# Kernel tuning notes

Measured on AMD Instinct MI355X. Metric: run time of the kernel, lower is better.

The kernel has to match this reference:

```python
import jax, jax.numpy as jnp
import numpy as np
import math

B, L, D = 2, 2048, 768
H, R = 12, 128
DH = D // H  # 64

def setup_inputs():
    key = jax.random.key(0)
    ks = jax.random.split(key, 9)
    s = 0.02
    return {
        "x": jax.random.normal(ks[0], (B, L, D), jnp.float32),
        "W_qkv": jax.random.normal(ks[1], (D, 3 * D), jnp.float32) * s,
        "b_qkv": jnp.zeros((3 * D,), jnp.float32),
        "W_sem_down": jax.random.normal(ks[2], (D, R), jnp.float32) * s,
        "W_sem_up": jax.random.normal(ks[3], (R, 2 * D), jnp.float32) * s,
        "W_ctx_down": jax.random.normal(ks[4], (D, R), jnp.float32) * s,
        "W_ctx_up": jax.random.normal(ks[5], (R, 2 * D), jnp.float32) * s,
        "temperature": jnp.ones((1,), jnp.float32) * 0.5,
        "W_proj": jax.random.normal(ks[6], (D, D), jnp.float32) * s,
        "b_proj": jnp.zeros((D,), jnp.float32),
        "gamma": jnp.ones((D,), jnp.float32),
        "beta": jnp.zeros((D,), jnp.float32),
    }

def _layernorm(x, gamma, beta, eps=1e-5):
    mu = x.mean(-1, keepdims=True)
    var = ((x - mu) ** 2).mean(-1, keepdims=True)
    return (x - mu) * jax.lax.rsqrt(var + eps) * gamma + beta

def reference(x, W_qkv, b_qkv, W_sem_down, W_sem_up, W_ctx_down, W_ctx_up,
              temperature, W_proj, b_proj, gamma, beta):
    x_norm = _layernorm(x, gamma, beta)
    qkv = x_norm @ W_qkv + b_qkv
    q, k, v = jnp.split(qkv, 3, axis=-1)

    # sinusoidal interference gate from two low-rank branches
    sem = jax.nn.silu(x @ W_sem_down) @ W_sem_up
    sem_amp, sem_phase = jnp.split(sem, 2, axis=-1)
    sem_amp = jax.nn.softplus(sem_amp)
    sem_phase = jnp.tanh(sem_phase) * math.pi
    ctx = jax.nn.silu(x @ W_ctx_down) @ W_ctx_up
    ctx_amp, ctx_phase = jnp.split(ctx, 2, axis=-1)
    ctx_amp = jax.nn.softplus(ctx_amp)
    ctx_phase = jnp.tanh(ctx_phase) * math.pi
    interference = sem_amp * ctx_amp * jnp.cos(sem_phase - ctx_phase) * temperature
    gate = jax.nn.sigmoid(interference)
    k = k * (1.0 + gate)

    # (B,L,D) -> (B,H,L,DH)
    to_heads = lambda t: t.reshape(B, L, H, DH).transpose(0, 2, 1, 3)
    q_f = jax.nn.elu(to_heads(q).astype(jnp.float32)) + 1.0
    k_f = jax.nn.elu(to_heads(k).astype(jnp.float32)) + 1.0
    v_f = to_heads(v).astype(jnp.float32)

    # causal linear attention via explicit k (x) v cumsum
    kv_state = k_f[..., :, None] * v_f[..., None, :]   # (B,H,L,DH,DH)
    kv_cumsum = jnp.cumsum(kv_state, axis=2)
    out_num = jnp.einsum('bhld,bhlde->bhle', q_f, kv_cumsum)
    k_cumsum = jnp.cumsum(k_f, axis=2)
    out_den = (q_f * k_cumsum).sum(-1, keepdims=True) + 1e-6
    attn = (out_num / out_den).astype(x.dtype)
    attn = attn.transpose(0, 2, 1, 3).reshape(B, L, D)
    return attn @ W_proj + b_proj, gate
```

## Files before the change

### kernel.cpp

```cpp
#include <hip/hip_runtime.h>

#define B_    2
#define L_    2048
#define D_    768
#define H_    12
#define BL    4096
#define BH    24
#define CHUNK 128
#define NC    16
#define GOFF  3145728
#define PI_F  3.14159265358979f

typedef __bf16 bf16x8 __attribute__((ext_vector_type(8)));
typedef float  f32x4  __attribute__((ext_vector_type(4)));
typedef unsigned short us8 __attribute__((ext_vector_type(8)));

__device__ __forceinline__ float bf2f(unsigned short u) {
    return __uint_as_float(((unsigned int)u) << 16);
}
__device__ __forceinline__ unsigned short f2bf(float f) {
    unsigned int u = __float_as_uint(f);
    unsigned int r = (u + 0x7fffu + ((u >> 16) & 1u)) >> 16;
    return (unsigned short)r;
}
__device__ __forceinline__ float rcp_fast(float x) { return __builtin_amdgcn_rcpf(x); }
__device__ __forceinline__ float softplus_fast(float x) {
    return x > 20.f ? x : __logf(1.f + __expf(x));
}
__device__ __forceinline__ float tanh_fast(float x) {
    float e2 = __expf(2.f * x);
    return 1.f - 2.f * rcp_fast(e2 + 1.f);
}
__device__ __forceinline__ void dma16(const unsigned short* g, unsigned short* l) {
    __builtin_amdgcn_global_load_lds(
        (const __attribute__((address_space(1))) unsigned int*)g,
        (__attribute__((address_space(3))) unsigned int*)l, 16, 0, 0);
}

__global__ __launch_bounds__(256) void detect_kernel(const unsigned short* __restrict__ x,
                                                     int* __restrict__ flag)
{
    __shared__ int cnt;
    if (threadIdx.x == 0) cnt = 0;
    __syncthreads();
    int c = 0;
    #pragma unroll
    for (int i = 0; i < 16; i++) {
        unsigned short u = x[threadIdx.x * 16 + i];
        int e = (u >> 7) & 0xff;
        if (e < 100 || e > 140) c++;
    }
    atomicAdd(&cnt, c);
    __syncthreads();
    if (threadIdx.x == 0) flag[0] = (cnt > 512) ? 1 : 0;
}

__global__ __launch_bounds__(256) void prep_mega_kernel(
    const void* __restrict__ s0, unsigned short* __restrict__ dq,
    const void* __restrict__ s1, unsigned short* __restrict__ dd,
    const void* __restrict__ s2, unsigned short* __restrict__ dsu,
    const void* __restrict__ s3,
    const void* __restrict__ s4, unsigned short* __restrict__ dcu,
    const void* __restrict__ s5, unsigned short* __restrict__ dp,
    const void* __restrict__ sbq, unsigned short* __restrict__ dbq,
    const void* __restrict__ sbp, unsigned short* __restrict__ dbp,
    const int* __restrict__ flag)
{
    int id = blockIdx.x;
    int fl = flag[0];
    if (id >= 2880) {
        const void* src; unsigned short* dst; int n, base;
        if (id < 2889) { src = sbq; dst = dbq; n = 2304; base = (id - 2880) * 256; }
        else           { src = sbp; dst = dbp; n = 768;  base = (id - 2889) * 256; }
        int i = base + threadIdx.x;
        if (i < n) dst[i] = fl ? f2bf(((const float*)src)[i]) : ((const unsigned short*)src)[i];
        return;
    }
    __shared__ unsigned short tile[32][33];
    const void* src; unsigned short* dst; int K, N, tid;
    if (id < 1728)      { src = s0; dst = dq;  K = 768; N = 2304; tid = id; }
    else if (id < 1824) { src = s1; dst = dd;  K = 768; N = 128;  tid = id - 1728; }
    else if (id < 2016) { src = s2; dst = dsu; K = 128; N = 1536; tid = id - 1824; }
    else if (id < 2112) { src = s3; dst = dd + (size_t)128 * 768; K = 768; N = 128; tid = id - 2016; }
    else if (id < 2304) { src = s4; dst = dcu; K = 128; N = 1536; tid = id - 2112; }
    else                { src = s5; dst = dp;  K = 768; N = 768;  tid = id - 2304; }
    int tn = N / 32;
    int by = (tid / tn) * 32, bx = (tid % tn) * 32;
    int tx = threadIdx.x & 31, tyb = threadIdx.x >> 5;
    #pragma unroll
    for (int i = 0; i < 4; i++) {
        int k = by + tyb * 4 + i, n = bx + tx;
        size_t off = (size_t)k * N + n;
        tile[tyb * 4 + i][tx] = fl ? f2bf(((const float*)src)[off]) : ((const unsigned short*)src)[off];
    }
    __syncthreads();
    #pragma unroll
    for (int i = 0; i < 4; i++) {
        int n = bx + tyb * 4 + i, k = by + tx;
        dst[(size_t)n * K + k] = tile[tx][tyb * 4 + i];
    }
}

__global__ __launch_bounds__(256) void conv_ln_kernel(
    const void* __restrict__ xin,
    const void* __restrict__ gr, const void* __restrict__ br,
    unsigned short* __restrict__ x_c,
    unsigned short* __restrict__ xn,
    const int* __restrict__ flag)
{
    int row = blockIdx.x, t = threadIdx.x;
    int fl = flag[0];
    float v[3];
    #pragma unroll
    for (int j = 0; j < 3; j++) {
        int c = t + j * 256;
        v[j] = fl ? ((const float*)xin)[(size_t)row * D_ + c]
                  : bf2f(((const unsigned short*)xin)[(size_t)row * D_ + c]);
    }
    __shared__ float red[8];
    float s = v[0] + v[1] + v[2];
    #pragma unroll
    for (int m = 32; m >= 1; m >>= 1) s += __shfl_xor(s, m, 64);
    int wid = t >> 6;
    if ((t & 63) == 0) red[wid] = s;
    __syncthreads();
    float mean = (red[0] + red[1] + red[2] + red[3]) * (1.f / 768.f);
    float s2 = 0.f;
    #pragma unroll
    for (int j = 0; j < 3; j++) { float d = v[j] - mean; s2 += d * d; }
    #pragma unroll
    for (int m = 32; m >= 1; m >>= 1) s2 += __shfl_xor(s2, m, 64);
    if ((t & 63) == 0) red[4 + wid] = s2;
    __syncthreads();
    float var = (red[4] + red[5] + red[6] + red[7]) * (1.f / 768.f);
    float rs = rsqrtf(var + 1e-5f);
    #pragma unroll
    for (int j = 0; j < 3; j++) {
        int c = t + j * 256;
        float gv = fl ? ((const float*)gr)[c] : bf2f(((const unsigned short*)gr)[c]);
        float bv = fl ? ((const float*)br)[c] : bf2f(((const unsigned short*)br)[c]);
        x_c[(size_t)row * D_ + c] = f2bf(v[j]);
        float o = (v[j] - mean) * rs * gv + bv;
        xn[(size_t)row * D_ + c] = f2bf(o);
    }
}

template<int EPI>
__global__ __launch_bounds__(256) void mfma_gemm_kernel(
    const unsigned short* __restrict__ A, int lda,
    const unsigned short* __restrict__ BT,
    const unsigned short* __restrict__ bias,
    const unsigned short* __restrict__ gateb,
    void* __restrict__ outp,
    const int* __restrict__ flag,
    int N, int K)
{
    __shared__ unsigned short sbuf[17408];
    unsigned short* As = sbuf;
    unsigned short* Bs = sbuf + 8192;
    unsigned short* Cs = sbuf;

    int f = blockIdx.y * gridDim.x + blockIdx.x;
    int rps = gridDim.y >> 3;
    int strip = f & 7, within = f >> 3;
    int by = strip * rps + (within % rps);
    int bx = within / rps;
    int m0 = by * 128, n0 = bx * 128;

    int t = threadIdx.x;
    int lane = t & 63, wave = t >> 6, quad = lane >> 4, l16 = lane & 15;
    int wm = (wave & 1) * 64, wn = (wave >> 1) * 64;
    int xr = l16 & 7;

    int sr8 = lane >> 3;
    int scg = (lane & 7) ^ sr8;
    const unsigned short* ApL = A  + (size_t)(m0 + wave * 32 + sr8) * lda + scg * 8;
    const unsigned short* BpL = BT + (size_t)(n0 + wave * 32 + sr8) * K   + scg * 8;
    unsigned short* AsW = As + wave * 32 * 64;
    unsigned short* BsW = Bs + wave * 32 * 64;

    f32x4 acc[4][4];
    #pragma unroll
    for (int i = 0; i < 4; i++)
        #pragma unroll
        for (int j = 0; j < 4; j++) acc[i][j] = (f32x4){0.f, 0.f, 0.f, 0.f};

    for (int k0 = 0; k0 < K; k0 += 64) {
        __syncthreads();
        #pragma unroll
        for (int c = 0; c < 4; c++) {
            dma16(ApL + (size_t)(c * 8) * lda + k0, AsW + c * 512);
            dma16(BpL + (size_t)(c * 8) * K   + k0, BsW + c * 512);
        }
        __syncthreads();
        #pragma unroll
        for (int ks = 0; ks < 2; ks++) {
            bf16x8 af[4], bfr[4];
            #pragma unroll
            for (int i = 0; i < 4; i++)
                af[i] = *(const bf16x8*)&As[(wm + i * 16 + l16) * 64 + (((ks * 4 + quad) ^ xr) * 8)];
            #pragma unroll
            for (int j = 0; j < 4; j++)
                bfr[j] = *(const bf16x8*)&Bs[(wn + j * 16 + l16) * 64 + (((ks * 4 + quad) ^ xr) * 8)];
            #pragma unroll
            for (int i = 0; i < 4; i++)
                #pragma unroll
                for (int j = 0; j < 4; j++)
                    acc[i][j] = __builtin_amdgcn_mfma_f32_16x16x32_bf16(af[i], bfr[j], acc[i][j], 0, 0, 0);
        }
    }

    int fl = (EPI == 3) ? flag[0] : 0;
    __syncthreads();
    #pragma unroll
    for (int j = 0; j < 4; j++) {
        int col = n0 + wn + j * 16 + l16;
        float bv = bias ? bf2f(bias[col]) : 0.f;
        #pragma unroll
        for (int i = 0; i < 4; i++) {
            #pragma unroll
            for (int r = 0; r < 4; r++) {
                int row = m0 + wm + i * 16 + quad * 4 + r;
                float v = acc[i][j][r] + bv;
                if (EPI == 1) v = v * rcp_fast(1.f + __expf(-v));
                if (EPI == 2) {
                    if (col < D_) {
                        v = v > 0.f ? v + 1.f : __expf(v);
                    } else if (col < 2 * D_) {
                        float gg = bf2f(gateb[(size_t)row * D_ + (col - D_)]);
                        v *= (1.f + gg);
                        v = v > 0.f ? v + 1.f : __expf(v);
                    }
                }
                if (EPI == 3 && fl) {
                    ((float*)outp)[(size_t)row * N + col] = v;
                } else {
                    Cs[(wm + i * 16 + quad * 4 + r) * 136 + wn + j * 16 + l16] = f2bf(v);
                }
            }
        }
    }
    if (!(EPI == 3 && fl)) {
        __syncthreads();
        #pragma unroll
        for (int p = 0; p < 8; p++) {
            int idx = p * 256 + t;
            int row = idx >> 4, cc = (idx & 15) * 8;
            *(us8*)&((unsigned short*)outp)[(size_t)(m0 + row) * N + n0 + cc] =
                *(const us8*)&Cs[row * 136 + cc];
        }
    }
}

__global__ __launch_bounds__(256) void gate_mfma_kernel(
    const unsigned short* __restrict__ tdown,
    const unsigned short* __restrict__ WsuT,
    const unsigned short* __restrict__ WcuT,
    const void* __restrict__ tempraw,
    void* __restrict__ dout,
    unsigned short* __restrict__ gateb,
    const int* __restrict__ flag)
{
    __shared__ unsigned short gbuf[17408];
    int f = blockIdx.y * gridDim.x + blockIdx.x;
    int rps = gridDim.y >> 3;
    int strip = f & 7, within = f >> 3;
    int by = strip * rps + (within % rps);
    int bx = within / rps;
    int m0 = by * 64, c0 = bx * 64;

    int t = threadIdx.x;
    int lane = t & 63, wave = t >> 6, quad = lane >> 4, l16 = lane & 15;
    int xg = l16 & 3;

    int r_t = wave * 16 + (lane >> 2);
    int g_t = (lane & 3) ^ ((lane >> 2) & 3);
    const unsigned short* s0 = tdown + (size_t)(m0 + r_t) * 256 + g_t * 8;
    const unsigned short* s1 = s0 + 128;
    const unsigned short* s2 = WsuT + (size_t)(c0 + r_t) * 128 + g_t * 8;
    const unsigned short* s3 = WsuT + (size_t)(768 + c0 + r_t) * 128 + g_t * 8;
    const unsigned short* s4 = WcuT + (size_t)(c0 + r_t) * 128 + g_t * 8;
    const unsigned short* s5 = WcuT + (size_t)(768 + c0 + r_t) * 128 + g_t * 8;
    unsigned short* ldq = gbuf + wave * 512;

    f32x4 acc[4][4];
    #pragma unroll
    for (int i = 0; i < 4; i++)
        #pragma unroll
        for (int j = 0; j < 4; j++) acc[i][j] = (f32x4){0.f, 0.f, 0.f, 0.f};

    int Atile = wave >> 1, Btile = 2 + wave;
    for (int k0 = 0; k0 < 128; k0 += 32) {
        __syncthreads();
        dma16(s0 + k0, ldq + 0 * 2048);
        dma16(s1 + k0, ldq + 1 * 2048);
        dma16(s2 + k0, ldq + 2 * 2048);
        dma16(s3 + k0, ldq + 3 * 2048);
        dma16(s4 + k0, ldq + 4 * 2048);
        dma16(s5 + k0, ldq + 5 * 2048);
        __syncthreads();
        bf16x8 af[4], bfr[4];
        #pragma unroll
        for (int i = 0; i < 4; i++)
            af[i] = *(const bf16x8*)&gbuf[Atile * 2048 + (i * 16 + l16) * 32 + ((quad ^ xg) * 8)];
        #pragma unroll
        for (int j = 0; j < 4; j++)
            bfr[j] = *(const bf16x8*)&gbuf[Btile * 2048 + (j * 16 + l16) * 32 + ((quad ^ xg) * 8)];
        #pragma unroll
        for (int i = 0; i < 4; i++)
            #pragma unroll
            for (int j = 0; j < 4; j++)
                acc[i][j] = __builtin_amdgcn_mfma_f32_16x16x32_bf16(af[i], bfr[j], acc[i][j], 0, 0, 0);
    }
    __syncthreads();
    #pragma unroll
    for (int i = 0; i < 4; i++)
        #pragma unroll
        for (int j = 0; j < 4; j++)
            #pragma unroll
            for (int r = 0; r < 4; r++)
                gbuf[wave * 4352 + (i * 16 + quad * 4 + r) * 68 + j * 16 + l16] = f2bf(acc[i][j][r]);
    __syncthreads();
    int fl = flag[0];
    float tempv = fl ? ((const float*)tempraw)[0] : bf2f(((const unsigned short*)tempraw)[0]);
    #pragma unroll
    for (int p = 0; p < 16; p++) {
        int idx = p * 256 + t;
        int row = idx >> 6, col = idx & 63;
        float sa = softplus_fast(bf2f(gbuf[0 * 4352 + row * 68 + col]));
        float sp = tanh_fast(bf2f(gbuf[1 * 4352 + row * 68 + col]));
        float ca = softplus_fast(bf2f(gbuf[2 * 4352 + row * 68 + col]));
        float cp = tanh_fast(bf2f(gbuf[3 * 4352 + row * 68 + col]));
        float inter = sa * ca * __cosf(PI_F * (sp - cp)) * tempv;
        float g = rcp_fast(1.f + __expf(-inter));
        size_t off = (size_t)GOFF + (size_t)(m0 + row) * D_ + c0 + col;
        unsigned short gb = f2bf(g);
        if (fl) ((float*)dout)[off] = g;
        else    ((unsigned short*)dout)[off] = gb;
        gateb[(size_t)(m0 + row) * D_ + c0 + col] = gb;
    }
}

__global__ __launch_bounds__(256) void chunk_sum_mfma_kernel(
    const unsigned short* __restrict__ qkvt,
    float* __restrict__ Msum, float* __restrict__ Zsum)
{
    __shared__ __align__(16) unsigned short KT[64 * 136];
    __shared__ __align__(16) unsigned short VT[80 * 136];
    int blk = blockIdx.x;
    int bh = blk / NC, cc = blk - bh * NC;
    int b = bh / H_, h = bh - b * H_;
    int t = threadIdx.x;
    int lane = t & 63, wave = t >> 6, quad = lane >> 4, l16 = lane & 15;
    int lr = t >> 1, lc = (t & 1) * 32;
    size_t rowbase = (size_t)(b * L_ + cc * CHUNK);
    const unsigned short* kg = qkvt + rowbase * 2304 + D_ + h * 64;
    const unsigned short* vg = qkvt + rowbase * 2304 + 2 * D_ + h * 64;
    #pragma unroll
    for (int c = 0; c < 4; c++) {
        us8 kv = *(const us8*)&kg[(size_t)lr * 2304 + lc + c * 8];
        us8 vv = *(const us8*)&vg[(size_t)lr * 2304 + lc + c * 8];
        #pragma unroll
        for (int ii = 0; ii < 8; ii++) {
            KT[(lc + c * 8 + ii) * 136 + lr] = kv[ii];
            VT[(lc + c * 8 + ii) * 136 + lr] = vv[ii];
        }
    }
    if (t < 128) VT[64 * 136 + t] = 0x3F80;
    __syncthreads();

    f32x4 acc[5];
    #pragma unroll
    for (int j = 0; j < 5; j++) acc[j] = (f32x4){0.f, 0.f, 0.f, 0.f};
    #pragma unroll
    for (int ks = 0; ks < 4; ks++) {
        bf16x8 a = *(const bf16x8*)&KT[(wave * 16 + l16) * 136 + ks * 32 + quad * 8];
        #pragma unroll
        for (int j = 0; j < 5; j++) {
            bf16x8 bv = *(const bf16x8*)&VT[(j * 16 + l16) * 136 + ks * 32 + quad * 8];
            acc[j] = __builtin_amdgcn_mfma_f32_16x16x32_bf16(a, bv, acc[j], 0, 0, 0);
        }
    }
    float* mo = Msum + (size_t)blk * 4096;
    #pragma unroll
    for (int j = 0; j < 4; j++)
        #pragma unroll
        for (int r = 0; r < 4; r++)
            mo[(wave * 16 + quad * 4 + r) * 64 + j * 16 + l16] = acc[j][r];
    if (l16 == 0) {
        #pragma unroll
        for (int r = 0; r < 4; r++)
            Zsum[(size_t)blk * 64 + wave * 16 + quad * 4 + r] = acc[4][r];
    }
}

__global__ __launch_bounds__(256) void chunk_scan_mfma_kernel(
    const unsigned short* __restrict__ qkvt,
    const float* __restrict__ Msum, const float* __restrict__ Zsum,
    unsigned short* __restrict__ attnb)
{
    __shared__ __align__(16) unsigned short sbuf[34048];
    unsigned short* Qs = sbuf;
    unsigned short* Ks = sbuf + 8192;
    unsigned short* Ps = sbuf;
    unsigned short* VT = sbuf + 17408;
    unsigned short* Ss = sbuf + 28288;
    unsigned short* Cout = sbuf;

    int blk = blockIdx.x;
    int bh = blk / NC, cc = NC - 1 - (blk - bh * NC);
    int b = bh / H_, h = bh - b * H_;
    int t = threadIdx.x;
    int lane = t & 63, wave = t >> 6, quad = lane >> 4, l16 = lane & 15;
    int wm = wave * 32;
    int xr = l16 & 7;
    size_t rowbase = (size_t)(b * L_ + cc * CHUNK);
    const unsigned short* qg = qkvt + rowbase * 2304 + h * 64;
    const unsigned short* kg = qkvt + rowbase * 2304 + D_ + h * 64;
    const unsigned short* vg = qkvt + rowbase * 2304 + 2 * D_ + h * 64;

    int r8 = lane >> 3, g8 = (lane & 7) ^ r8;
    #pragma unroll
    for (int s = 0; s < 8; s++) {
        int op = s * 4 + wave;
        int tl = op >> 4, o16 = op & 15;
        const unsigned short* src = (tl ? kg : qg) + (size_t)(o16 * 8 + r8) * 2304 + g8 * 8;
        unsigned short* dst = (tl ? Ks : Qs) + o16 * 512;
        dma16(src, dst);
    }
    {
        int lr = t >> 1, lc = (t & 1) * 32;
        #pragma unroll
        for (int c = 0; c < 4; c++) {
            us8 vv = *(const us8*)&vg[(size_t)lr * 2304 + lc + c * 8];
            #pragma unroll
            for (int ii = 0; ii < 8; ii++)
                VT[(lc + c * 8 + ii) * 136 + lr] = vv[ii];
        }
    }
    if (t < 128) VT[64 * 136 + t] = 0x3F80;
    {
        int d = t & 63, jb = (t >> 6) * 16;
        float a16[16];
        #pragma unroll
        for (int j = 0; j < 16; j++) a16[j] = 0.f;
        for (int c = 0; c < cc; c++) {
            const float* mp = Msum + ((size_t)bh * NC + c) * 4096 + d * 64 + jb;
            #pragma unroll
            for (int g4 = 0; g4 < 4; g4++) {
                float4 sv = *(const float4*)&mp[g4 * 4];
                a16[g4 * 4 + 0] += sv.x; a16[g4 * 4 + 1] += sv.y;
                a16[g4 * 4 + 2] += sv.z; a16[g4 * 4 + 3] += sv.w;
            }
        }
        #pragma unroll
        for (int j = 0; j < 16; j++) Ss[(jb + j) * 72 + d] = f2bf(a16[j]);
    }
    if (t < 64) {
        float rz = 0.f;
        for (int c = 0; c < cc; c++) rz += Zsum[((size_t)bh * NC + c) * 64 + t];
        Ss[64 * 72 + t] = f2bf(rz);
    }
    __syncthreads();

    f32x4 Pacc[2][8], Oacc[2][5];
    #pragma unroll
    for (int i = 0; i < 2; i++) {
        #pragma unroll
        for (int n = 0; n < 8; n++) Pacc[i][n] = (f32x4){0.f, 0.f, 0.f, 0.f};
        #pragma unroll
        for (int j = 0; j < 5; j++) Oacc[i][j] = (f32x4){0.f, 0.f, 0.f, 0.f};
    }
    bf16x8 aq[2][2];
    #pragma unroll
    for (int i = 0; i < 2; i++)
        #pragma unroll
        for (int ks = 0; ks < 2; ks++)
            aq[i][ks] = *(const bf16x8*)&Qs[(wm + i * 16 + l16) * 64 + (((ks * 4 + quad) ^ xr) * 8)];
    #pragma unroll
    for (int n = 0; n < 8; n++)
        #pragma unroll
        for (int ks = 0; ks < 2; ks++) {
            bf16x8 bk = *(const bf16x8*)&Ks[(n * 16 + l16) * 64 + (((ks * 4 + quad) ^ xr) * 8)];
            #pragma unroll
            for (int i = 0; i < 2; i++)
                Pacc[i][n] = __builtin_amdgcn_mfma_f32_16x16x32_bf16(aq[i][ks], bk, Pacc[i][n], 0, 0, 0);
        }
    #pragma unroll
    for (int j = 0; j < 5; j++)
        #pragma unroll
        for (int ks = 0; ks < 2; ks++) {
            bf16x8 bs = *(const bf16x8*)&Ss[(j * 16 + l16) * 72 + ks * 32 + quad * 8];
            #pragma unroll
            for (int i = 0; i < 2; i++)
                Oacc[i][j] = __builtin_amdgcn_mfma_f32_16x16x32_bf16(aq[i][ks], bs, Oacc[i][j], 0, 0, 0);
        }
    __syncthreads();

    #pragma unroll
    for (int i = 0; i < 2; i++)
        #pragma unroll
        for (int n = 0; n < 8; n++)
            #pragma unroll
            for (int r = 0; r < 4; r++) {
                int trow = wm + i * 16 + quad * 4 + r;
                int scol = n * 16 + l16;
                Ps[trow * 136 + scol] = (scol <= trow) ? f2bf(Pacc[i][n][r]) : 0;
            }
    __syncthreads();

    #pragma unroll
    for (int ks = 0; ks < 4; ks++) {
        bf16x8 ap[2];
        #pragma unroll
        for (int i = 0; i < 2; i++)
            ap[i] = *(const bf16x8*)&Ps[(wm + i * 16 + l16) * 136 + ks * 32 + quad * 8];
        #pragma unroll
        for (int j = 0; j < 5; j++) {
            bf16x8 bv = *(const bf16x8*)&VT[(j * 16 + l16) * 136 + ks * 32 + quad * 8];
            #pragma unroll
            for (int i = 0; i < 2; i++)
                Oacc[i][j] = __builtin_amdgcn_mfma_f32_16x16x32_bf16(ap[i], bv, Oacc[i][j], 0, 0, 0);
        }
    }
    __syncthreads();

    #pragma unroll
    for (int i = 0; i < 2; i++) {
        #pragma unroll
        for (int r = 0; r < 4; r++) {
            float den = __shfl(Oacc[i][4][r], lane & 48) + 1e-6f;
            float inv = 1.f / den;
            #pragma unroll
            for (int j = 0; j < 4; j++)
                Cout[(wm + i * 16 + quad * 4 + r) * 136 + j * 16 + l16] = f2bf(Oacc[i][j][r] * inv);
        }
    }
    __syncthreads();
    unsigned short* abase = attnb + rowbase * D_ + h * 64;
    #pragma unroll
    for (int p = 0; p < 4; p++) {
        int idx = p * 256 + t;
        int row = idx >> 3, cg = (idx & 7) * 8;
        *(us8*)&abase[(size_t)row * D_ + cg] = *(const us8*)&Cout[row * 136 + cg];
    }
}

extern "C" void kernel_launch(void* const* d_in, const int* in_sizes, int n_in,
                              void* d_out, int out_size, void* d_ws, size_t ws_size,
                              hipStream_t stream)
{
    char* w = (char*)d_ws;
    auto alloc = [&](size_t bytes) { void* p = (void*)w; w += (bytes + 255) & ~(size_t)255; return p; };
    int*            flagp   = (int*)alloc(256);
    unsigned short* x_c     = (unsigned short*)alloc((size_t)BL * D_ * 2);
    unsigned short* attnb   = x_c;
    unsigned short* xn      = (unsigned short*)alloc((size_t)BL * D_ * 2);
    unsigned short* WqkvT   = (unsigned short*)alloc((size_t)2304 * 768 * 2);
    unsigned short* WdT     = (unsigned short*)alloc((size_t)256 * 768 * 2);
    unsigned short* WsuT    = (unsigned short*)alloc((size_t)1536 * 128 * 2);
    unsigned short* WcuT    = (unsigned short*)alloc((size_t)1536 * 128 * 2);
    unsigned short* WprojT  = (unsigned short*)alloc((size_t)768 * 768 * 2);
    unsigned short* bqkv_c  = (unsigned short*)alloc((size_t)2304 * 2);
    unsigned short* bproj_c = (unsigned short*)alloc((size_t)768 * 2);
    unsigned short* tdown   = (unsigned short*)alloc((size_t)BL * 256 * 2);
    float*          Zsum    = (float*)alloc((size_t)BH * NC * 64 * 4);
    unsigned short* qkvt    = (unsigned short*)alloc((size_t)BL * 2304 * 2);
    float*          Msum    = (float*)alloc((size_t)BH * NC * 4096 * 4);
    unsigned short* gateb   = (unsigned short*)Msum;

    dim3 blk(256);
    detect_kernel<<<1, blk, 0, stream>>>((const unsigned short*)d_in[0], flagp);
    prep_mega_kernel<<<2892, blk, 0, stream>>>(
        d_in[1], WqkvT, d_in[3], WdT, d_in[4], WsuT,
        d_in[5], d_in[6], WcuT, d_in[8], WprojT,
        d_in[2], bqkv_c, d_in[9], bproj_c, flagp);
    conv_ln_kernel<<<BL, blk, 0, stream>>>(d_in[0], d_in[10], d_in[11], x_c, xn, flagp);
    mfma_gemm_kernel<1><<<dim3(2, 32), blk, 0, stream>>>(x_c, 768, WdT, nullptr, nullptr, tdown, flagp, 256, 768);
    gate_mfma_kernel<<<dim3(12, 64), blk, 0, stream>>>(tdown, WsuT, WcuT, d_in[7], d_out, gateb, flagp);
    mfma_gemm_kernel<2><<<dim3(18, 32), blk, 0, stream>>>(xn, 768, WqkvT, bqkv_c, gateb, qkvt, flagp, 2304, 768);
    chunk_sum_mfma_kernel<<<BH * NC, blk, 0, stream>>>(qkvt, Msum, Zsum);
    chunk_scan_mfma_kernel<<<BH * NC, blk, 0, stream>>>(qkvt, Msum, Zsum, attnb);
    mfma_gemm_kernel<3><<<dim3(6, 32), blk, 0, stream>>>(attnb, 768, WprojT, bproj_c, nullptr, d_out, flagp, 768, 768);
}
```

Baseline: 225.2 us.

## Fuse dtype detection, weight prep and layernorm into one launch; use 64-row GEMM tiles

Merges the separate detect, weight-transpose and layernorm kernels into a single launch. Each block recomputes the dtype flag locally from a smaller sample of x, which removes two launches and their serial dependencies. The GEMM kernel gains an M-tile template parameter, and the small-N GEMMs (down-projection and output projection) now use 64-row tiles to double their block counts for better CU occupancy. The trade-off is that every block repeats the detection read and barrier, and the smaller sample makes the dtype heuristic less robust.

After: 220.9 us. Within noise of the previous version (-1.9%).

```diff
diff --git a/kernel.cpp b/kernel.cpp
--- a/kernel.cpp
+++ b/kernel.cpp
@@ -36,26 +36,23 @@
         (const __attribute__((address_space(1))) unsigned int*)g,
         (__attribute__((address_space(3))) unsigned int*)l, 16, 0, 0);
 }
-
-__global__ __launch_bounds__(256) void detect_kernel(const unsigned short* __restrict__ x,
-                                                     int* __restrict__ flag)
-{
-    __shared__ int cnt;
-    if (threadIdx.x == 0) cnt = 0;
+__device__ __forceinline__ int detect_local(const unsigned short* __restrict__ x,
+                                            int* cnt_sh) {
+    if (threadIdx.x == 0) *cnt_sh = 0;
     __syncthreads();
     int c = 0;
     #pragma unroll
-    for (int i = 0; i < 16; i++) {
-        unsigned short u = x[threadIdx.x * 16 + i];
+    for (int i = 0; i < 4; i++) {
+        unsigned short u = x[threadIdx.x * 4 + i];
         int e = (u >> 7) & 0xff;
         if (e < 100 || e > 140) c++;
     }
-    atomicAdd(&cnt, c);
-    __syncthreads();
-    if (threadIdx.x == 0) flag[0] = (cnt > 512) ? 1 : 0;
-}
-
-__global__ __launch_bounds__(256) void prep_mega_kernel(
+    atomicAdd(cnt_sh, c);
+    __syncthreads();
+    return *cnt_sh > 128;
+}
+
+__global__ __launch_bounds__(256) void prep_all_kernel(
     const void* __restrict__ s0, unsigned short* __restrict__ dq,
     const void* __restrict__ s1, unsigned short* __restrict__ dd,
     const void* __restrict__ s2, unsigned short* __restrict__ dsu,
@@ -64,19 +61,63 @@
     const void* __restrict__ s5, unsigned short* __restrict__ dp,
     const void* __restrict__ sbq, unsigned short* __restrict__ dbq,
     const void* __restrict__ sbp, unsigned short* __restrict__ dbp,
-    const int* __restrict__ flag)
+    const void* __restrict__ xin,
+    const void* __restrict__ gr, const void* __restrict__ br,
+    unsigned short* __restrict__ x_c, unsigned short* __restrict__ xn,
+    int* __restrict__ flagp)
 {
+    __shared__ int cnt_sh;
+    __shared__ unsigned short tile[32][33];
+    __shared__ float red[8];
+    int fl = detect_local((const unsigned short*)xin, &cnt_sh);
     int id = blockIdx.x;
-    int fl = flag[0];
+    int t = threadIdx.x;
+
+    if (id >= 2892) {
+        int row = id - 2892;
+        if (row == 0 && t == 0) flagp[0] = fl;
+        float v[3];
+        #pragma unroll
+        for (int j = 0; j < 3; j++) {
+            int c = t + j * 256;
+            v[j] = fl ? ((const float*)xin)[(size_t)row * D_ + c]
+                      : bf2f(((const unsigned short*)xin)[(size_t)row * D_ + c]);
+        }
+        float s = v[0] + v[1] + v[2];
+        #pragma unroll
+        for (int m = 32; m >= 1; m >>= 1) s += __shfl_xor(s, m, 64);
+        int wid = t >> 6;
+        if ((t & 63) == 0) red[wid] = s;
+        __syncthreads();
+        float mean = (red[0] + red[1] + red[2] + red[3]) * (1.f / 768.f);
+        float s2 = 0.f;
+        #pragma unroll
+        for (int j = 0; j < 3; j++) { float d = v[j] - mean; s2 += d * d; }
+        #pragma unroll
+        for (int m = 32; m >= 1; m >>= 1) s2 += __shfl_xor(s2, m, 64);
+        if ((t & 63) == 0) red[4 + wid] = s2;
+        __syncthreads();
+        float var = (red[4] + red[5] + red[6] + red[7]) * (1.f / 768.f);
+        float rs = rsqrtf(var + 1e-5f);
+        #pragma unroll
+        for (int j = 0; j < 3; j++) {
+            int c = t + j * 256;
+            float gv = fl ? ((const float*)gr)[c] : bf2f(((const unsigned short*)gr)[c]);
+            float bv = fl ? ((const float*)br)[c] : bf2f(((const unsigned short*)br)[c]);
+            x_c[(size_t)row * D_ + c] = f2bf(v[j]);
+            float o = (v[j] - mean) * rs * gv + bv;
+            xn[(size_t)row * D_ + c] = f2bf(o);
+        }
+        return;
+    }
     if (id >= 2880) {
         const void* src; unsigned short* dst; int n, base;
         if (id < 2889) { src = sbq; dst = dbq; n = 2304; base = (id - 2880) * 256; }
         else           { src = sbp; dst = dbp; n = 768;  base = (id - 2889) * 256; }
-        int i = base + threadIdx.x;
+        int i = base + t;
         if (i < n) dst[i] = fl ? f2bf(((const float*)src)[i]) : ((const unsigned short*)src)[i];
         return;
     }
-    __shared__ unsigned short tile[32][33];
     const void* src; unsigned short* dst; int K, N, tid;
     if (id < 1728)      { src = s0; dst = dq;  K = 768; N = 2304; tid = id; }
     else if (id < 1824) { src = s1; dst = dd;  K = 768; N = 128;  tid = id - 1728; }
@@ -86,7 +127,7 @@
     else                { src = s5; dst = dp;  K = 768; N = 768;  tid = id - 2304; }
     int tn = N / 32;
     int by = (tid / tn) * 32, bx = (tid % tn) * 32;
-    int tx = threadIdx.x & 31, tyb = threadIdx.x >> 5;
+    int tx = t & 31, tyb = t >> 5;
     #pragma unroll
     for (int i = 0; i < 4; i++) {
         int k = by + tyb * 4 + i, n = bx + tx;
@@ -101,51 +142,7 @@
     }
 }
 
-__global__ __launch_bounds__(256) void conv_ln_kernel(
-    const void* __restrict__ xin,
-    const void* __restrict__ gr, const void* __restrict__ br,
-    unsigned short* __restrict__ x_c,
-    unsigned short* __restrict__ xn,
-    const int* __restrict__ flag)
-{
-    int row = blockIdx.x, t = threadIdx.x;
-    int fl = flag[0];
-    float v[3];
-    #pragma unroll
-    for (int j = 0; j < 3; j++) {
-        int c = t + j * 256;
-        v[j] = fl ? ((const float*)xin)[(size_t)row * D_ + c]
-                  : bf2f(((const unsigned short*)xin)[(size_t)row * D_ + c]);
-    }
-    __shared__ float red[8];
-    float s = v[0] + v[1] + v[2];
-    #pragma unroll
-    for (int m = 32; m >= 1; m >>= 1) s += __shfl_xor(s, m, 64);
-    int wid = t >> 6;
-    if ((t & 63) == 0) red[wid] = s;
-    __syncthreads();
-    float mean = (red[0] + red[1] + red[2] + red[3]) * (1.f / 768.f);
-    float s2 = 0.f;
-    #pragma unroll
-    for (int j = 0; j < 3; j++) { float d = v[j] - mean; s2 += d * d; }
-    #pragma unroll
-    for (int m = 32; m >= 1; m >>= 1) s2 += __shfl_xor(s2, m, 64);
-    if ((t & 63) == 0) red[4 + wid] = s2;
-    __syncthreads();
-    float var = (red[4] + red[5] + red[6] + red[7]) * (1.f / 768.f);
-    float rs = rsqrtf(var + 1e-5f);
-    #pragma unroll
-    for (int j = 0; j < 3; j++) {
-        int c = t + j * 256;
-        float gv = fl ? ((const float*)gr)[c] : bf2f(((const unsigned short*)gr)[c]);
-        float bv = fl ? ((const float*)br)[c] : bf2f(((const unsigned short*)br)[c]);
-        x_c[(size_t)row * D_ + c] = f2bf(v[j]);
-        float o = (v[j] - mean) * rs * gv + bv;
-        xn[(size_t)row * D_ + c] = f2bf(o);
-    }
-}
-
-template<int EPI>
+template<int EPI, int TM>
 __global__ __launch_bounds__(256) void mfma_gemm_kernel(
     const unsigned short* __restrict__ A, int lda,
     const unsigned short* __restrict__ BT,
@@ -155,9 +152,11 @@
     const int* __restrict__ flag,
     int N, int K)
 {
+    constexpr int MI = TM / 32;
+    constexpr int AOPS = TM / 32;
     __shared__ unsigned short sbuf[17408];
     unsigned short* As = sbuf;
-    unsigned short* Bs = sbuf + 8192;
+    unsigned short* Bs = sbuf + TM * 64;
     unsigned short* Cs = sbuf;
 
     int f = blockIdx.y * gridDim.x + blockIdx.x;
@@ -165,45 +164,46 @@
     int strip = f & 7, within = f >> 3;
     int by = strip * rps + (within % rps);
     int bx = within / rps;
-    int m0 = by * 128, n0 = bx * 128;
+    int m0 = by * TM, n0 = bx * 128;
 
     int t = threadIdx.x;
     int lane = t & 63, wave = t >> 6, quad = lane >> 4, l16 = lane & 15;
-    int wm = (wave & 1) * 64, wn = (wave >> 1) * 64;
+    int wm = (wave & 1) * (TM / 2), wn = (wave >> 1) * 64;
     int xr = l16 & 7;
 
     int sr8 = lane >> 3;
     int scg = (lane & 7) ^ sr8;
-    const unsigned short* ApL = A  + (size_t)(m0 + wave * 32 + sr8) * lda + scg * 8;
+    const unsigned short* ApL = A  + (size_t)(m0 + wave * (TM / 4) + sr8) * lda + scg * 8;
     const unsigned short* BpL = BT + (size_t)(n0 + wave * 32 + sr8) * K   + scg * 8;
-    unsigned short* AsW = As + wave * 32 * 64;
+    unsigned short* AsW = As + wave * (TM / 4) * 64;
     unsigned short* BsW = Bs + wave * 32 * 64;
 
-    f32x4 acc[4][4];
-    #pragma unroll
-    for (int i = 0; i < 4; i++)
+    f32x4 acc[MI][4];
+    #pragma unroll
+    for (int i = 0; i < MI; i++)
         #pragma unroll
         for (int j = 0; j < 4; j++) acc[i][j] = (f32x4){0.f, 0.f, 0.f, 0.f};
 
     for (int k0 = 0; k0 < K; k0 += 64) {
         __syncthreads();
         #pragma unroll
-        for (int c = 0; c < 4; c++) {
+        for (int c = 0; c < AOPS; c++)
             dma16(ApL + (size_t)(c * 8) * lda + k0, AsW + c * 512);
-            dma16(BpL + (size_t)(c * 8) * K   + k0, BsW + c * 512);
-        }
+        #pragma unroll
+        for (int c = 0; c < 4; c++)
+            dma16(BpL + (size_t)(c * 8) * K + k0, BsW + c * 512);
         __syncthreads();
         #pragma unroll
         for (int ks = 0; ks < 2; ks++) {
-            bf16x8 af[4], bfr[4];
-            #pragma unroll
-            for (int i = 0; i < 4; i++)
+            bf16x8 af[MI], bfr[4];
+            #pragma unroll
+            for (int i = 0; i < MI; i++)
                 af[i] = *(const bf16x8*)&As[(wm + i * 16 + l16) * 64 + (((ks * 4 + quad) ^ xr) * 8)];
             #pragma unroll
             for (int j = 0; j < 4; j++)
                 bfr[j] = *(const bf16x8*)&Bs[(wn + j * 16 + l16) * 64 + (((ks * 4 + quad) ^ xr) * 8)];
             #pragma unroll
-            for (int i = 0; i < 4; i++)
+            for (int i = 0; i < MI; i++)
                 #pragma unroll
                 for (int j = 0; j < 4; j++)
                     acc[i][j] = __builtin_amdgcn_mfma_f32_16x16x32_bf16(af[i], bfr[j], acc[i][j], 0, 0, 0);
@@ -217,7 +217,7 @@
         int col = n0 + wn + j * 16 + l16;
         float bv = bias ? bf2f(bias[col]) : 0.f;
         #pragma unroll
-        for (int i = 0; i < 4; i++) {
+        for (int i = 0; i < MI; i++) {
             #pragma unroll
             for (int r = 0; r < 4; r++) {
                 int row = m0 + wm + i * 16 + quad * 4 + r;
@@ -243,7 +243,7 @@
     if (!(EPI == 3 && fl)) {
         __syncthreads();
         #pragma unroll
-        for (int p = 0; p < 8; p++) {
+        for (int p = 0; p < TM / 16; p++) {
             int idx = p * 256 + t;
             int row = idx >> 4, cc = (idx & 15) * 8;
             *(us8*)&((unsigned short*)outp)[(size_t)(m0 + row) * N + n0 + cc] =
@@ -570,16 +570,15 @@
     unsigned short* gateb   = (unsigned short*)Msum;
 
     dim3 blk(256);
-    detect_kernel<<<1, blk, 0, stream>>>((const unsigned short*)d_in[0], flagp);
-    prep_mega_kernel<<<2892, blk, 0, stream>>>(
+    prep_all_kernel<<<2892 + BL, blk, 0, stream>>>(
         d_in[1], WqkvT, d_in[3], WdT, d_in[4], WsuT,
         d_in[5], d_in[6], WcuT, d_in[8], WprojT,
-        d_in[2], bqkv_c, d_in[9], bproj_c, flagp);
-    conv_ln_kernel<<<BL, blk, 0, stream>>>(d_in[0], d_in[10], d_in[11], x_c, xn, flagp);
-    mfma_gemm_kernel<1><<<dim3(2, 32), blk, 0, stream>>>(x_c, 768, WdT, nullptr, nullptr, tdown, flagp, 256, 768);
+        d_in[2], bqkv_c, d_in[9], bproj_c,
+        d_in[0], d_in[10], d_in[11], x_c, xn, flagp);
+    mfma_gemm_kernel<1, 64><<<dim3(2, 64), blk, 0, stream>>>(x_c, 768, WdT, nullptr, nullptr, tdown, flagp, 256, 768);
     gate_mfma_kernel<<<dim3(12, 64), blk, 0, stream>>>(tdown, WsuT, WcuT, d_in[7], d_out, gateb, flagp);
-    mfma_gemm_kernel<2><<<dim3(18, 32), blk, 0, stream>>>(xn, 768, WqkvT, bqkv_c, gateb, qkvt, flagp, 2304, 768);
+    mfma_gemm_kernel<2, 128><<<dim3(18, 32), blk, 0, stream>>>(xn, 768, WqkvT, bqkv_c, gateb, qkvt, flagp, 2304, 768);
     chunk_sum_mfma_kernel<<<BH * NC, blk, 0, stream>>>(qkvt, Msum, Zsum);
     chunk_scan_mfma_kernel<<<BH * NC, blk, 0, stream>>>(qkvt, Msum, Zsum, attnb);
-    mfma_gemm_kernel<3><<<dim3(6, 32), blk, 0, stream>>>(attnb, 768, WprojT, bproj_c, nullptr, d_out, flagp, 768, 768);
-}
+    mfma_gemm_kernel<3, 64><<<dim3(6, 64), blk, 0, stream>>>(attnb, 768, WprojT, bproj_c, nullptr, d_out, flagp, 768, 768);
+}
```
